# Optimization experiments

Hardware: AMD Instinct MI355X
Metric: run time of the kernel (lower is better)

The kernel has to match this reference:

```python
import jax, jax.numpy as jnp
import numpy as np
from jax import lax
from jax.scipy.special import logsumexp

B, T, Lc = 64, 512, 16
DW, CD, NF, KS, H, K, CV = 300, 50, 100, 3, 256, 9, 100
SCALE = 0.05


def setup_inputs() -> dict:
    key = jax.random.key(0)
    ks = jax.random.split(key, 20)
    f32 = jnp.float32
    return {
        'word_embs': jax.random.normal(ks[0], (B, T, DW), f32),
        'chars': jax.random.randint(ks[1], (B, T, Lc), 0, CV),
        'lengths': jax.random.randint(ks[2], (B,), T // 2, T + 1).astype(jnp.int32),
        'tags': jax.random.randint(ks[3], (B, T), 0, K),
        'fin_W': jax.random.normal(ks[4], (DW, DW), f32) * SCALE,
        'fin_b': jnp.zeros((DW,), f32),
        'char_emb': jax.random.normal(ks[5], (CV, CD), f32) * SCALE,
        'conv_W': jax.random.normal(ks[6], (KS, CD, NF), f32) * SCALE,  # (W, In, Out)
        'conv_b': jnp.zeros((NF,), f32),
        'Wih_f': jax.random.normal(ks[7], (4 * H, DW + NF), f32) * SCALE,
        'Whh_f': jax.random.normal(ks[8], (4 * H, H), f32) * SCALE,
        'b_f': jnp.zeros((4 * H,), f32),
        'Wih_b': jax.random.normal(ks[9], (4 * H, DW + NF), f32) * SCALE,
        'Whh_b': jax.random.normal(ks[10], (4 * H, H), f32) * SCALE,
        'b_b': jnp.zeros((4 * H,), f32),
        'out_W': jax.random.normal(ks[11], (2 * H, K), f32) * SCALE,
        'out_b': jnp.zeros((K,), f32),
        'trans': jax.random.normal(ks[12], (K, K), f32) * SCALE,
        'start_trans': jax.random.normal(ks[13], (K,), f32) * SCALE,
        'end_trans': jax.random.normal(ks[14], (K,), f32) * SCALE,
    }


def _lstm_scan(x, mask, Wih, Whh, b):
    # x: [B,T,D], mask: [B,T] bool -> outputs [B,T,H] (zeros at padding)
    xT = jnp.swapaxes(x, 0, 1)              # [T,B,D]
    mT = jnp.swapaxes(mask, 0, 1)           # [T,B]
    pre = jnp.einsum('tbd,gd->tbg', xT, Wih) + b  # precompute input part [T,B,4H]
    h0 = jnp.zeros((x.shape[0], Whh.shape[1]), x.dtype)

    def step(carry, inp):
        h, c = carry
        px, m = inp
        g = px + h @ Whh.T
        i, f, gg, o = jnp.split(g, 4, axis=-1)  # pytorch gate order i,f,g,o
        c_new = jax.nn.sigmoid(f) * c + jax.nn.sigmoid(i) * jnp.tanh(gg)
        h_new = jax.nn.sigmoid(o) * jnp.tanh(c_new)
        m = m[:, None]
        h2 = jnp.where(m, h_new, h)
        c2 = jnp.where(m, c_new, c)
        return (h2, c2), h2 * m

    _, hs = lax.scan(step, (h0, h0), (pre, mT))
    return jnp.swapaxes(hs, 0, 1)


def _reverse_by_length(x, lengths):
    # reverse the valid prefix of each sequence (padding stays at the end)
    t = jnp.arange(x.shape[1])
    rev = jnp.where(t[None, :] < lengths[:, None], lengths[:, None] - 1 - t[None, :], t[None, :])
    return jnp.take_along_axis(x, rev[:, :, None], axis=1)


def _crf_forward(logits, tags, mask, trans, start_trans, end_trans):
    # torchcrf-style log-likelihood; returns scalar sum over batch
    eT = jnp.swapaxes(logits, 0, 1)  # [T,B,K]
    mT = jnp.swapaxes(mask, 0, 1).astype(logits.dtype)  # [T,B]
    bidx = jnp.arange(logits.shape[0])
    # numerator: gold path score
    score = start_trans[tags[:, 0]] + eT[0][bidx, tags[:, 0]]

    def nstep(carry, inp):
        sc, prev = carry
        e, tg, m = inp
        step_sc = trans[prev, tg] + e[bidx, tg]
        sc = sc + m * step_sc
        prev = jnp.where(m > 0, tg, prev)
        return (sc, prev), None

    tT = jnp.swapaxes(tags, 0, 1)
    (score, last_tag), _ = lax.scan(nstep, (score, tags[:, 0]), (eT[1:], tT[1:], mT[1:]))
    score = score + end_trans[last_tag]
    # denominator: log-partition via forward algorithm
    alpha = start_trans[None, :] + eT[0]

    def fstep(a, inp):
        e, m = inp
        nxt = logsumexp(a[:, :, None] + trans[None, :, :] + e[:, None, :], axis=1)
        return jnp.where(m[:, None] > 0, nxt, a), None

    alpha, _ = lax.scan(fstep, alpha, (eT[1:], mT[1:]))
    Z = logsumexp(alpha + end_trans[None, :], axis=-1)
    return jnp.sum(score - Z)


def _viterbi(logits, mask, trans, start_trans, end_trans):
    eT = jnp.swapaxes(logits, 0, 1)  # [T,B,K]
    mT = jnp.swapaxes(mask, 0, 1)    # [T,B] bool
    Ktags = logits.shape[-1]
    ident = jnp.arange(Ktags)[None, :]

    def vstep(a, inp):
        e, m = inp
        cand = a[:, :, None] + trans[None, :, :]   # [B, K_prev, K_cur]
        bp = jnp.argmax(cand, axis=1)
        nxt = jnp.max(cand, axis=1) + e
        a2 = jnp.where(m[:, None], nxt, a)
        bp = jnp.where(m[:, None], bp, ident)       # identity backptr at padding
        return a2, bp

    alpha, bps = lax.scan(vstep, start_trans[None, :] + eT[0], (eT[1:], mT[1:]))
    last = jnp.argmax(alpha + end_trans[None, :], axis=-1)

    def bstep(tag, bp):
        prev = jnp.take_along_axis(bp, tag[:, None], axis=1)[:, 0]
        return prev, tag

    tag0, tail = lax.scan(bstep, last, bps, reverse=True)  # tail[t] = tag at time t+1
    path = jnp.concatenate([tag0[:, None], jnp.swapaxes(tail, 0, 1)], axis=1)  # [B,T]
    return path * mask  # zero-pad like zero_pad(preds)


def reference(word_embs, chars, lengths, tags, fin_W, fin_b, char_emb, conv_W, conv_b,
              Wih_f, Whh_f, b_f, Wih_b, Whh_b, b_b, out_W, out_b,
              trans, start_trans, end_trans):
    mask = jnp.arange(T)[None, :] < lengths[:, None]  # [B,T]
    # 1) word embeddings through finetune linear
    we = word_embs @ fin_W.T + fin_b
    # 2) char CNN: embed -> conv1d over chars -> relu -> max-pool
    ce = char_emb[chars].reshape(B * T, Lc, CD)
    conv = lax.conv_general_dilated(ce, conv_W, (1,), 'SAME',
                                    dimension_numbers=('NWC', 'WIO', 'NWC')) + conv_b
    char_feat = jnp.max(jax.nn.relu(conv), axis=1).reshape(B, T, NF)
    # 3) concat; 4) BiLSTM (dropout=0 / eval mode)
    x = jnp.concatenate([we, char_feat], axis=-1)
    h_fwd = _lstm_scan(x, mask, Wih_f, Whh_f, b_f)
    x_rev = _reverse_by_length(x, lengths)
    h_bwd = _reverse_by_length(_lstm_scan(x_rev, mask, Wih_b, Whh_b, b_b), lengths)
    lstm_out = jnp.concatenate([h_fwd, h_bwd], axis=-1)  # [B,T,2H]
    # 5) linear head; 6-7) CRF loss + viterbi decode
    logits = lstm_out @ out_W + out_b  # [B,T,K]
    loss = -_crf_forward(logits, tags, mask, trans, start_trans, end_trans)
    preds = _viterbi(logits, mask, trans, start_trans, end_trans)
    return loss, preds
```

## Files before the change

### kernel.cpp

```cpp
#include <hip/hip_runtime.h>


__device__ __forceinline__ float sigf(float x){ return 1.0f/(1.0f + expf(-x)); }

__global__ void pack_weights(const float* __restrict__ Wih_f, const float* __restrict__ Wih_b,
                             const float* __restrict__ Whh_f, const float* __restrict__ Whh_b,
                             const float* __restrict__ fin_W,
                             float4* __restrict__ Wp_f, float4* __restrict__ Wp_b,
                             float4* __restrict__ WT_f, float4* __restrict__ WT_b,
                             float* __restrict__ finWT){
  int stride = gridDim.x*blockDim.x;
  for (int idx = blockIdx.x*blockDim.x + threadIdx.x; idx < 425872; idx += stride){
    if (idx < 204800){
      int i2 = idx; const float* W = Wih_f; float4* P = Wp_f;
      if (i2 >= 102400){ i2 -= 102400; W = Wih_b; P = Wp_b; }
      int d = i2 >> 8, j = i2 & 255;
      P[i2] = make_float4(W[j*400+d], W[(j+256)*400+d], W[(j+512)*400+d], W[(j+768)*400+d]);
    } else if (idx < 335872){
      int i2 = idx - 204800; const float* W = Whh_f; float4* P = WT_f;
      if (i2 >= 65536){ i2 -= 65536; W = Whh_b; P = WT_b; }
      int d = i2 >> 8, j = i2 & 255;
      P[i2] = make_float4(W[j*256+d], W[(j+256)*256+d], W[(j+512)*256+d], W[(j+768)*256+d]);
    } else {
      int i2 = idx - 335872;
      int d = i2 / 300, j = i2 - d*300;
      finWT[d*304 + j] = fin_W[j*300 + d];
    }
  }
}

__global__ __launch_bounds__(256) void featurize(const float* __restrict__ we_in,
      const float* __restrict__ finWT, const float* __restrict__ finb,
      const int* __restrict__ chars, const float* __restrict__ char_emb,
      const float* __restrict__ convW, const float* __restrict__ convb,
      float* __restrict__ x){
  __shared__ __align__(16) char fsm[31104];
  int bid = blockIdx.x;
  int tid = threadIdx.x;
  if (bid < 2048){
    float* embT = (float*)fsm;
    int tok0 = bid * 16;
    for (int idx = tid; idx < 4800; idx += 256){
      int tt = idx / 300, d = idx - tt*300;
      embT[d*16 + tt] = we_in[(size_t)tok0*300 + idx];
    }
    __syncthreads();
    for (int j = tid; j < 300; j += 256){
      float bias = finb[j];
      float acc[16];
#pragma unroll
      for (int k2=0;k2<16;k2++) acc[k2]=bias;
      const float4* e4 = (const float4*)embT;
#pragma unroll 4
      for (int d=0; d<300; d++){
        float w = finWT[d*304 + j];
        float4 a = e4[d*4+0], b2 = e4[d*4+1], c2 = e4[d*4+2], d2 = e4[d*4+3];
        acc[0]+=a.x*w;  acc[1]+=a.y*w;  acc[2]+=a.z*w;  acc[3]+=a.w*w;
        acc[4]+=b2.x*w; acc[5]+=b2.y*w; acc[6]+=b2.z*w; acc[7]+=b2.w*w;
        acc[8]+=c2.x*w; acc[9]+=c2.y*w; acc[10]+=c2.z*w;acc[11]+=c2.w*w;
        acc[12]+=d2.x*w;acc[13]+=d2.y*w;acc[14]+=d2.z*w;acc[15]+=d2.w*w;
      }
#pragma unroll
      for (int k2=0;k2<16;k2++) x[(size_t)(tok0+k2)*400 + j] = acc[k2];
    }
  } else {
    float* ce2 = (float*)fsm;
    int* chs = (int*)(fsm + 30464);
    int tok0 = (bid - 2048) * 8;
    if (tid < 128) chs[tid] = chars[(size_t)tok0*16 + tid];
    __syncthreads();
    for (int idx = tid; idx < 7200; idx += 256){
      int tok = idx / 900; int r = idx - tok*900;
      int w1 = r / 50; int c = r - w1*50;
      float v = 0.f;
      if (w1 >= 1 && w1 <= 16) v = char_emb[chs[tok*16 + (w1-1)]*50 + c];
      ce2[tok*952 + c*19 + w1] = v;
    }
    __syncthreads();
    for (int p = tid; p < 800; p += 256){
      int tok = p / 100, f = p - tok*100;
      float s[16];
#pragma unroll
      for (int w=0; w<16; w++) s[w] = 0.f;
      const float* cebase = ce2 + tok*952;
      for (int c=0; c<50; c++){
        float cr[18];
#pragma unroll
        for (int i=0;i<18;i++) cr[i] = cebase[c*19+i];
#pragma unroll
        for (int k2=0;k2<3;k2++){
          float wv = convW[(k2*50+c)*100 + f];
#pragma unroll
          for (int w=0;w<16;w++) s[w] += cr[w+k2]*wv;
        }
      }
      float m = s[0];
#pragma unroll
      for (int w=1;w<16;w++) m = fmaxf(m, s[w]);
      m = fmaxf(0.f, m + convb[f]);
      x[(size_t)(tok0+tok)*400 + 300 + f] = m;
    }
  }
}

__global__ __launch_bounds__(256) void pre_gemm(const float* __restrict__ x,
     const float4* __restrict__ Wp_f, const float4* __restrict__ Wp_b,
     const float* __restrict__ b_f, const float* __restrict__ b_b,
     const int* __restrict__ lengths,
     float4* __restrict__ pre_f, float4* __restrict__ pre_b,
     int t0, int log2CH){
  int dir = blockIdx.z;
  const float4* Wp = dir ? Wp_b : Wp_f;
  const float* bias = dir ? b_b : b_f;
  float4* pre = dir ? pre_b : pre_f;
  int tok0 = blockIdx.x * 64;
  int j0 = blockIdx.y * 64;
  __shared__ float As[16][68];
  __shared__ float4 Bs[4][16][16];
  __shared__ int rows_s[64];
  int tid = threadIdx.x;
  int tx = tid & 15, ty = tid >> 4;
  int chm = (1 << log2CH) - 1;
  if (tid < 64){
    int tok = tok0 + tid;
    int b = tok >> log2CH;
    int trel = tok & chm;
    int t = t0 + trel;
    int row;
    if (dir == 0) row = t;
    else { int len = lengths[b]; int pr = len - 1 - t; row = pr < 0 ? 0 : pr; }
    rows_s[tid] = b*512 + row;
  }
  float4 acc[4][4];
#pragma unroll
  for (int s2=0;s2<4;s2++){
    int j = j0 + tx*4 + s2;
    float4 bj = make_float4(bias[j], bias[j+256], bias[j+512], bias[j+768]);
#pragma unroll
    for (int r=0;r<4;r++) acc[r][s2] = bj;
  }
  __syncthreads();
  int tokA = tid >> 2, kqA = tid & 3;
  int jjB = tid & 63,  kbB = tid >> 6;
  float4 aReg; float4 bReg[4];
  {
    aReg = *(const float4*)&x[(size_t)rows_s[tokA]*400 + 0 + kqA*4];
#pragma unroll
    for (int rr=0;rr<4;rr++) bReg[rr] = Wp[(size_t)(0 + kbB + rr*4)*256 + j0 + jjB];
  }
  for (int kt=0; kt<25; ++kt){
    As[kqA*4+0][tokA] = aReg.x;
    As[kqA*4+1][tokA] = aReg.y;
    As[kqA*4+2][tokA] = aReg.z;
    As[kqA*4+3][tokA] = aReg.w;
#pragma unroll
    for (int rr=0;rr<4;rr++) Bs[jjB&3][kbB+rr*4][jjB>>2] = bReg[rr];
    __syncthreads();
    if (kt < 24){
      int k0n = (kt+1)*16;
      aReg = *(const float4*)&x[(size_t)rows_s[tokA]*400 + k0n + kqA*4];
#pragma unroll
      for (int rr=0;rr<4;rr++) bReg[rr] = Wp[(size_t)(k0n + kbB + rr*4)*256 + j0 + jjB];
    }
#pragma unroll
    for (int kk=0; kk<16; ++kk){
      float a[4];
#pragma unroll
      for (int r=0;r<4;r++) a[r] = As[kk][ty*4+r];
#pragma unroll
      for (int s2=0;s2<4;s2++){
        float4 b4 = Bs[s2][kk][tx];
#pragma unroll
        for (int r=0;r<4;r++){
          acc[r][s2].x += a[r]*b4.x;
          acc[r][s2].y += a[r]*b4.y;
          acc[r][s2].z += a[r]*b4.z;
          acc[r][s2].w += a[r]*b4.w;
        }
      }
    }
    __syncthreads();
  }
#pragma unroll
  for (int r=0;r<4;r++){
    int tok = tok0 + ty*4 + r;
    int bb = tok >> log2CH;
    int tr = tok & chm;
#pragma unroll
    for (int s2=0;s2<4;s2++){
      pre[(size_t)(bb*128 + tr)*256 + j0 + tx*4 + s2] = acc[r][s2];
    }
  }
}

#define NRD 24
#define NLD 8
#define NSTREAM (64 - NRD - NLD)

#define OFF_WLDS 0
#define OFF_PART 131072
#define OFF_OWS  143360
#define OFF_H    152576
#define POOL_SZ  154624
#define PG_AS    0
#define PG_BS    4352
#define PG_ROWS  12544
#define PG_STRIDE 12800

__global__ __attribute__((amdgpu_num_vgpr(128))) __launch_bounds__(1024, 1)
void fused_scan_pre(const float4* __restrict__ prec_f, const float4* __restrict__ prec_b,
     const float4* __restrict__ pren_f, float4* __restrict__ pren_f_w,
     float4* __restrict__ pren_b_w,
     const float4* __restrict__ WT_f, const float4* __restrict__ WT_b,
     const float4* __restrict__ Wp_f, const float4* __restrict__ Wp_b,
     const float* __restrict__ b_f, const float* __restrict__ b_b,
     const float* __restrict__ x, const int* __restrict__ lengths,
     const float* __restrict__ outW,
     float* __restrict__ logits_f, float* __restrict__ logits_b,
     float* __restrict__ st_h, float* __restrict__ st_c,
     int t0, int nsteps, int t0n, int do_pre){
  __shared__ __align__(16) char smem[POOL_SZ];
  int wid = blockIdx.x;
  int tid = threadIdx.x;
  if (wid < 128){
    int dir = wid & 1;
    int b = wid >> 1;
    int len = lengths[b];
    if (len <= t0) return;
    const float4* pre = (dir ? prec_b : prec_f) + (size_t)b*128*256;
    const float4* WT = dir ? WT_b : WT_f;
    float* lg = (dir ? logits_b : logits_f) + (size_t)b*512*9;
    float4* wlds = (float4*)(smem + OFF_WLDS);
    float4* part = (float4*)(smem + OFF_PART);
    float*  oWs  = (float*)(smem + OFF_OWS);
    float*  hbuf = (float*)(smem + OFF_H);
    int j = tid & 255, q = tid >> 8;
    for (int i = tid; i < 2304; i += 1024) oWs[i] = outW[dir*2304 + i];
    for (int i = tid; i < 4*NLD*256; i += 1024){
      int qq = i >> 11;
      int rr = i & (NLD*256 - 1);
      int dl = rr >> 8, jj = rr & 255;
      wlds[(qq*NLD + dl)*256 + jj] = WT[(size_t)(qq*64 + NRD + dl)*256 + jj];
    }
    const float4* WTq = WT + (size_t)q*64*256;
    float4 wreg[NRD];
#pragma unroll
    for (int r=0; r<NRD; ++r) wreg[r] = WTq[(size_t)r*256 + j];
    float c = 0.f;
    if (t0 == 0){
      if (tid < 256) hbuf[tid] = 0.f;
    } else {
      if (tid < 256) hbuf[tid] = st_h[(dir*64+b)*256 + tid];
      if (q == 0) c = st_c[(dir*64+b)*256 + j];
    }
    __syncthreads();
    int tend = len < t0+nsteps ? len : t0+nsteps;
    const float4* WTs = WTq + (size_t)(NRD+NLD)*256 + j;
    int cur = 0;
    for (int t=t0; t<tend; ++t){
      const float* hc = hbuf + (cur << 8);
      const float* hq = hc + (q << 6);
      float4 p0;
      if (q == 0) p0 = pre[(size_t)(t - t0)*256 + j];
      float4 acc = make_float4(0.f,0.f,0.f,0.f);
#pragma unroll 8
      for (int s=0; s<NSTREAM; ++s){
        float hv = hq[NRD+NLD+s];
        float4 w = WTs[(size_t)s*256];
        acc.x += w.x*hv; acc.y += w.y*hv; acc.z += w.z*hv; acc.w += w.w*hv;
      }
#pragma unroll
      for (int r=0; r<NRD; ++r){
        float hv = hq[r];
        float4 w = wreg[r];
        acc.x += w.x*hv; acc.y += w.y*hv; acc.z += w.z*hv; acc.w += w.w*hv;
      }
#pragma unroll
      for (int l=0; l<NLD; ++l){
        float hv = hq[NRD+l];
        float4 w = wlds[(q*NLD + l)*256 + j];
        acc.x += w.x*hv; acc.y += w.y*hv; acc.z += w.z*hv; acc.w += w.w*hv;
      }
      if (q) part[((q-1)<<8) + j] = acc;
      if (t > t0 && tid < 576){
        int pprev = dir ? (len - t) : (t - 1);
        int k = tid >> 6, l = tid & 63;
        float s = hc[l]*oWs[l*9+k] + hc[l+64]*oWs[(l+64)*9+k]
                + hc[l+128]*oWs[(l+128)*9+k] + hc[l+192]*oWs[(l+192)*9+k];
#pragma unroll
        for (int o=32; o; o>>=1) s += __shfl_down(s, o, 64);
        if (l == 0) lg[pprev*9 + k] = s;
      }
      __syncthreads();
      if (q == 0){
        float4 p1 = part[j], p2 = part[256+j], p3 = part[512+j];
        float gi = acc.x + p0.x + p1.x + p2.x + p3.x;
        float gf = acc.y + p0.y + p1.y + p2.y + p3.y;
        float gg = acc.z + p0.z + p1.z + p2.z + p3.z;
        float go = acc.w + p0.w + p1.w + p2.w + p3.w;
        c = sigf(gf)*c + sigf(gi)*tanhf(gg);
        float h = sigf(go)*tanhf(c);
        hbuf[((cur^1)<<8) + j] = h;
      }
      __syncthreads();
      cur ^= 1;
    }
    const float* hc = hbuf + (cur << 8);
    if (tid < 576){
      int plast = dir ? (len - tend) : (tend - 1);
      int k = tid >> 6, l = tid & 63;
      float s = hc[l]*oWs[l*9+k] + hc[l+64]*oWs[(l+64)*9+k]
              + hc[l+128]*oWs[(l+128)*9+k] + hc[l+192]*oWs[(l+192)*9+k];
#pragma unroll
      for (int o=32; o; o>>=1) s += __shfl_down(s, o, 64);
      if (l == 0) lg[plast*9 + k] = s;
    }
    if (tid < 256) st_h[(dir*64+b)*256 + tid] = hc[tid];
    if (q == 0) st_c[(dir*64+b)*256 + j] = c;
  } else {
    if (!do_pre) return;
    int w = wid - 128;
    int g = tid >> 8, lt = tid & 255;
    char* gp = smem + g*PG_STRIDE;
    float (*As)[68] = (float(*)[68])(gp + PG_AS);
    float4* Bsl = (float4*)(gp + PG_BS);
    int* rows = (int*)(gp + PG_ROWS);
    int tx = lt & 15, ty4 = (lt >> 4) * 4;
    int tokA = lt >> 2, kqA = lt & 3;
    int uB = lt & 31, kbB = lt >> 5;
    for (int s=0; s<4; ++s){
      int tix = s*512 + g*128 + w;
      int dir = tix & 1;
      int jh = (tix >> 1) & 7;
      int tokT = tix >> 4;
      int j0u = jh * 32;
      int tok0 = tokT * 64;
      const float4* Wp = dir ? Wp_b : Wp_f;
      const float* bias = dir ? b_b : b_f;
      float4* pren = dir ? pren_b_w : pren_f_w;
      __syncthreads();
      if (lt < 64){
        int tok = tok0 + lt;
        int bb = tok >> 7, trel = tok & 127;
        int t = t0n + trel; if (t > 511) t = 511;
        int row;
        if (dir == 0) row = t;
        else { int len = lengths[bb]; int pr = len - 1 - t; row = pr < 0 ? 0 : pr; }
        rows[lt] = bb*512 + row;
      }
      float4 acc[4][2];
#pragma unroll
      for (int s2=0;s2<2;s2++){
        int u = j0u + tx + s2*16;
        float4 bj = make_float4(bias[u], bias[u+256], bias[u+512], bias[u+768]);
#pragma unroll
        for (int r=0;r<4;r++) acc[r][s2] = bj;
      }
      __syncthreads();
      for (int kt=0; kt<25; ++kt){
        int k0 = kt*16;
        {
          const float* xr = x + (size_t)rows[tokA]*400 + k0 + kqA*4;
          float4 av = *(const float4*)xr;
          As[kqA*4+0][tokA]=av.x; As[kqA*4+1][tokA]=av.y;
          As[kqA*4+2][tokA]=av.z; As[kqA*4+3][tokA]=av.w;
          Bsl[kbB*32 + uB]     = Wp[(size_t)(k0+kbB)*256 + j0u + uB];
          Bsl[(kbB+8)*32 + uB] = Wp[(size_t)(k0+kbB+8)*256 + j0u + uB];
        }
        __syncthreads();
#pragma unroll 4
        for (int kk=0; kk<16; ++kk){
          float a0 = As[kk][ty4+0], a1 = As[kk][ty4+1], a2 = As[kk][ty4+2], a3 = As[kk][ty4+3];
          float4 b0 = Bsl[kk*32 + tx], b1 = Bsl[kk*32 + tx + 16];
          acc[0][0].x += a0*b0.x; acc[0][0].y += a0*b0.y; acc[0][0].z += a0*b0.z; acc[0][0].w += a0*b0.w;
          acc[1][0].x += a1*b0.x; acc[1][0].y += a1*b0.y; acc[1][0].z += a1*b0.z; acc[1][0].w += a1*b0.w;
          acc[2][0].x += a2*b0.x; acc[2][0].y += a2*b0.y; acc[2][0].z += a2*b0.z; acc[2][0].w += a2*b0.w;
          acc[3][0].x += a3*b0.x; acc[3][0].y += a3*b0.y; acc[3][0].z += a3*b0.z; acc[3][0].w += a3*b0.w;
          acc[0][1].x += a0*b1.x; acc[0][1].y += a0*b1.y; acc[0][1].z += a0*b1.z; acc[0][1].w += a0*b1.w;
          acc[1][1].x += a1*b1.x; acc[1][1].y += a1*b1.y; acc[1][1].z += a1*b1.z; acc[1][1].w += a1*b1.w;
          acc[2][1].x += a2*b1.x; acc[2][1].y += a2*b1.y; acc[2][1].z += a2*b1.z; acc[2][1].w += a2*b1.w;
          acc[3][1].x += a3*b1.x; acc[3][1].y += a3*b1.y; acc[3][1].z += a3*b1.z; acc[3][1].w += a3*b1.w;
        }
        __syncthreads();
      }
#pragma unroll
      for (int r=0;r<4;r++){
        int tok = tok0 + ty4 + r;
        pren[(size_t)tok*256 + j0u + tx]      = acc[r][0];
        pren[(size_t)tok*256 + j0u + tx + 16] = acc[r][1];
      }
    }
  }
}

__global__ __launch_bounds__(64) void crf_viterbi_kernel(const float* __restrict__ logits_f,
     const float* __restrict__ logits_b, const float* __restrict__ outb_,
     const int* __restrict__ tags, const int* __restrict__ lengths,
     const float* __restrict__ trans, const float* __restrict__ start_trans,
     const float* __restrict__ end_trans, float* __restrict__ loss_partial,
     float* __restrict__ preds){
  int wid = blockIdx.x;
  int is_crf = wid < 64 ? 1 : 0;
  int b = is_crf ? wid : wid - 64;
  int len = lengths[b];
  int tid = threadIdx.x;
  __shared__ float e_s[4608];
  __shared__ float tr[81];
  __shared__ float alpha[9];
  __shared__ int tg[512];
  __shared__ unsigned char bp[4608];
  const float* lf = logits_f + (size_t)b*4608;
  const float* lb = logits_b + (size_t)b*4608;
  for (int i=tid; i<4608; i+=64){
    int k = i - (i/9)*9;
    e_s[i] = lf[i] + lb[i] + outb_[k];
  }
  for (int i=tid; i<81; i+=64) tr[i] = trans[i];
  if (is_crf){
    for (int i=tid; i<512; i+=64) tg[i] = tags[b*512 + i];
    __syncthreads();
    if (tid < 9) alpha[tid] = start_trans[tid] + e_s[tid];
    __syncthreads();
    for (int t=1; t<len; ++t){
      float nxt = 0.f;
      if (tid < 9){
        float v[9];
#pragma unroll
        for (int j2=0;j2<9;j2++) v[j2] = alpha[j2] + tr[j2*9+tid];
        float m = v[0];
#pragma unroll
        for (int j2=1;j2<9;j2++) m = fmaxf(m, v[j2]);
        float ssum = 0.f;
#pragma unroll
        for (int j2=0;j2<9;j2++) ssum += expf(v[j2]-m);
        nxt = m + logf(ssum) + e_s[t*9+tid];
      }
      __syncthreads();
      if (tid < 9) alpha[tid] = nxt;
      __syncthreads();
    }
    if (tid == 0){
      float m = alpha[0] + end_trans[0];
      for (int k2=1;k2<9;k2++) m = fmaxf(m, alpha[k2]+end_trans[k2]);
      float ssum = 0.f;
      for (int k2=0;k2<9;k2++) ssum += expf(alpha[k2]+end_trans[k2]-m);
      float Z = m + logf(ssum);
      int prev = tg[0];
      float sc = start_trans[prev] + e_s[prev];
      for (int t=1;t<len;++t){
        int cur = tg[t];
        sc += tr[prev*9+cur] + e_s[t*9+cur];
        prev = cur;
      }
      sc += end_trans[prev];
      loss_partial[b] = Z - sc;
    }
  } else {
    __syncthreads();
    if (tid < 9) alpha[tid] = start_trans[tid] + e_s[tid];
    __syncthreads();
    for (int t=1; t<len; ++t){
      float nxt = 0.f; int bj = 0;
      if (tid < 9){
        float m = alpha[0] + tr[tid];
#pragma unroll
        for (int j2=1;j2<9;j2++){
          float v = alpha[j2] + tr[j2*9+tid];
          if (v > m){ m = v; bj = j2; }
        }
        nxt = m + e_s[t*9+tid];
      }
      __syncthreads();
      if (tid < 9){ alpha[tid] = nxt; bp[t*9+tid] = (unsigned char)bj; }
      __syncthreads();
    }
    for (int p2 = len + tid; p2 < 512; p2 += 64) preds[(size_t)b*512 + p2] = 0.f;
    if (tid == 0){
      float m = alpha[0] + end_trans[0]; int last = 0;
      for (int k2=1;k2<9;k2++){
        float v = alpha[k2] + end_trans[k2];
        if (v > m){ m = v; last = k2; }
      }
      int cur = last;
      preds[(size_t)b*512 + (len-1)] = (float)cur;
      for (int p2 = len-2; p2 >= 0; --p2){
        cur = bp[(p2+1)*9 + cur];
        preds[(size_t)b*512 + p2] = (float)cur;
      }
    }
  }
}

__global__ void loss_sum_kernel(const float* __restrict__ lp, float* __restrict__ out){
  float v = lp[threadIdx.x];
#pragma unroll
  for (int o=32; o; o>>=1) v += __shfl_down(v, o, 64);
  if (threadIdx.x == 0) out[0] = v;
}

extern "C" void kernel_launch(void* const* d_in, const int* in_sizes, int n_in,
                              void* d_out, int out_size, void* d_ws, size_t ws_size,
                              hipStream_t stream) {
  const float* word_embs  = (const float*)d_in[0];
  const int*   chars      = (const int*)  d_in[1];
  const int*   lengths    = (const int*)  d_in[2];
  const int*   tags       = (const int*)  d_in[3];
  const float* fin_W      = (const float*)d_in[4];
  const float* fin_b      = (const float*)d_in[5];
  const float* char_emb   = (const float*)d_in[6];
  const float* conv_W     = (const float*)d_in[7];
  const float* conv_b     = (const float*)d_in[8];
  const float* Wih_f      = (const float*)d_in[9];
  const float* Whh_f      = (const float*)d_in[10];
  const float* b_f        = (const float*)d_in[11];
  const float* Wih_b      = (const float*)d_in[12];
  const float* Whh_b      = (const float*)d_in[13];
  const float* b_b        = (const float*)d_in[14];
  const float* out_W      = (const float*)d_in[15];
  const float* out_b      = (const float*)d_in[16];
  const float* trans      = (const float*)d_in[17];
  const float* start_tr   = (const float*)d_in[18];
  const float* end_tr     = (const float*)d_in[19];

  float* ws = (float*)d_ws;
  float*  x         = ws;
  float4* Wp_f      = (float4*)(ws + 13107200);
  float4* Wp_b      = (float4*)(ws + 13516800);
  float4* WT_f      = (float4*)(ws + 13926400);
  float4* WT_b      = (float4*)(ws + 14188544);
  float*  finWT     = ws + 14450688;
  float*  logits_f  = ws + 14541888;
  float*  logits_b  = ws + 14836800;
  float*  st_h      = ws + 15131712;
  float*  st_c      = ws + 15164480;
  float*  loss_part = ws + 15197248;
  const size_t FIXED_F = 15197312;
  float4* preA_f = (float4*)(ws + FIXED_F);
  float4* preA_b = preA_f + (size_t)64*128*256;
  float4* preB_f = preA_b + (size_t)64*128*256;
  float4* preB_b = preB_f + (size_t)64*128*256;

  float* out = (float*)d_out;

  pack_weights<<<1664, 256, 0, stream>>>(Wih_f, Wih_b, Whh_f, Whh_b, fin_W,
                                         Wp_f, Wp_b, WT_f, WT_b, finWT);
  featurize<<<6144, 256, 0, stream>>>(word_embs, finWT, fin_b, chars, char_emb,
                                      conv_W, conv_b, x);

  pre_gemm<<<dim3(32, 4, 2), 256, 0, stream>>>(x, Wp_f, Wp_b, b_f, b_b, lengths,
                                               preA_f, preA_b, 0, 5);
  fused_scan_pre<<<256, 1024, 0, stream>>>(preA_f, preA_b, preB_f, preB_f, preB_b,
      WT_f, WT_b, Wp_f, Wp_b, b_f, b_b, x, lengths, out_W,
      logits_f, logits_b, st_h, st_c, 0, 32, 32, 1);
  fused_scan_pre<<<256, 1024, 0, stream>>>(preB_f, preB_b, preA_f, preA_f, preA_b,
      WT_f, WT_b, Wp_f, Wp_b, b_f, b_b, x, lengths, out_W,
      logits_f, logits_b, st_h, st_c, 32, 128, 160, 1);
  fused_scan_pre<<<256, 1024, 0, stream>>>(preA_f, preA_b, preB_f, preB_f, preB_b,
      WT_f, WT_b, Wp_f, Wp_b, b_f, b_b, x, lengths, out_W,
      logits_f, logits_b, st_h, st_c, 160, 128, 288, 1);
  fused_scan_pre<<<256, 1024, 0, stream>>>(preB_f, preB_b, preA_f, preA_f, preA_b,
      WT_f, WT_b, Wp_f, Wp_b, b_f, b_b, x, lengths, out_W,
      logits_f, logits_b, st_h, st_c, 288, 128, 416, 1);
  fused_scan_pre<<<256, 1024, 0, stream>>>(preA_f, preA_b, preB_f, preB_f, preB_b,
      WT_f, WT_b, Wp_f, Wp_b, b_f, b_b, x, lengths, out_W,
      logits_f, logits_b, st_h, st_c, 416, 96, 0, 0);

  crf_viterbi_kernel<<<128, 64, 0, stream>>>(logits_f, logits_b, out_b, tags, lengths,
                                             trans, start_tr, end_tr, loss_part, out + 1);
  loss_sum_kernel<<<1, 64, 0, stream>>>(loss_part, out);
}
```

Measured before the change: 3.887 ms.

## Rebalance LSTM scan chunks so precompute GEMM hides behind each scan segment

Replaces the uneven 32/128/128/128/96 time-chunk schedule with six roughly equal 85/86-step chunks. The next chunk's input-projection GEMM now runs on the spare blocks during every scan launch instead of being exposed at the start, and works with chunk sizes that are not powers of two through an explicit output-position table. It also vectorises the shared-memory A-operand reads and drops the forced 128-VGPR cap on the fused kernel. The cost is an extra kernel launch, integer division in the index math, and a possible register-pressure change.

```diff
diff --git a/kernel.cpp b/kernel.cpp
--- a/kernel.cpp
+++ b/kernel.cpp
@@ -108,7 +108,7 @@
      const float* __restrict__ b_f, const float* __restrict__ b_b,
      const int* __restrict__ lengths,
      float4* __restrict__ pre_f, float4* __restrict__ pre_b,
-     int t0, int log2CH){
+     int t0, int CH){
   int dir = blockIdx.z;
   const float4* Wp = dir ? Wp_b : Wp_f;
   const float* bias = dir ? b_b : b_f;
@@ -118,18 +118,19 @@
   __shared__ float As[16][68];
   __shared__ float4 Bs[4][16][16];
   __shared__ int rows_s[64];
+  __shared__ int poss_s[64];
   int tid = threadIdx.x;
   int tx = tid & 15, ty = tid >> 4;
-  int chm = (1 << log2CH) - 1;
   if (tid < 64){
     int tok = tok0 + tid;
-    int b = tok >> log2CH;
-    int trel = tok & chm;
+    int b = tok / CH;
+    int trel = tok - b*CH;
     int t = t0 + trel;
     int row;
     if (dir == 0) row = t;
     else { int len = lengths[b]; int pr = len - 1 - t; row = pr < 0 ? 0 : pr; }
     rows_s[tid] = b*512 + row;
+    poss_s[tid] = b*128 + trel;
   }
   float4 acc[4][4];
 #pragma unroll
@@ -164,9 +165,8 @@
     }
 #pragma unroll
     for (int kk=0; kk<16; ++kk){
-      float a[4];
-#pragma unroll
-      for (int r=0;r<4;r++) a[r] = As[kk][ty*4+r];
+      float4 a4 = *(const float4*)&As[kk][ty*4];
+      float a[4] = {a4.x, a4.y, a4.z, a4.w};
 #pragma unroll
       for (int s2=0;s2<4;s2++){
         float4 b4 = Bs[s2][kk][tx];
@@ -183,12 +183,10 @@
   }
 #pragma unroll
   for (int r=0;r<4;r++){
-    int tok = tok0 + ty*4 + r;
-    int bb = tok >> log2CH;
-    int tr = tok & chm;
+    int pp = poss_s[ty*4+r];
 #pragma unroll
     for (int s2=0;s2<4;s2++){
-      pre[(size_t)(bb*128 + tr)*256 + j0 + tx*4 + s2] = acc[r][s2];
+      pre[(size_t)pp*256 + j0 + tx*4 + s2] = acc[r][s2];
     }
   }
 }
@@ -205,12 +203,11 @@
 #define PG_AS    0
 #define PG_BS    4352
 #define PG_ROWS  12544
-#define PG_STRIDE 12800
-
-__global__ __attribute__((amdgpu_num_vgpr(128))) __launch_bounds__(1024, 1)
+#define PG_STRIDE 13056
+
+__global__ __launch_bounds__(1024, 1)
 void fused_scan_pre(const float4* __restrict__ prec_f, const float4* __restrict__ prec_b,
-     const float4* __restrict__ pren_f, float4* __restrict__ pren_f_w,
-     float4* __restrict__ pren_b_w,
+     float4* __restrict__ pren_f_w, float4* __restrict__ pren_b_w,
      const float4* __restrict__ WT_f, const float4* __restrict__ WT_b,
      const float4* __restrict__ Wp_f, const float4* __restrict__ Wp_b,
      const float* __restrict__ b_f, const float* __restrict__ b_b,
@@ -218,7 +215,7 @@
      const float* __restrict__ outW,
      float* __restrict__ logits_f, float* __restrict__ logits_b,
      float* __restrict__ st_h, float* __restrict__ st_c,
-     int t0, int nsteps, int t0n, int do_pre){
+     int t0, int nsteps, int t0n, int cnext, int do_pre){
   __shared__ __align__(16) char smem[POOL_SZ];
   int wid = blockIdx.x;
   int tid = threadIdx.x;
@@ -325,11 +322,15 @@
     float (*As)[68] = (float(*)[68])(gp + PG_AS);
     float4* Bsl = (float4*)(gp + PG_BS);
     int* rows = (int*)(gp + PG_ROWS);
+    int* poss = rows + 64;
     int tx = lt & 15, ty4 = (lt >> 4) * 4;
     int tokA = lt >> 2, kqA = lt & 3;
     int uB = lt & 31, kbB = lt >> 5;
-    for (int s=0; s<4; ++s){
+    int tixmax = cnext << 4;
+    int smax = (tixmax + 511) >> 9;
+    for (int s=0; s<smax; ++s){
       int tix = s*512 + g*128 + w;
+      bool active = tix < tixmax;
       int dir = tix & 1;
       int jh = (tix >> 1) & 7;
       int tokT = tix >> 4;
@@ -339,14 +340,16 @@
       const float* bias = dir ? b_b : b_f;
       float4* pren = dir ? pren_b_w : pren_f_w;
       __syncthreads();
-      if (lt < 64){
+      if (active && lt < 64){
         int tok = tok0 + lt;
-        int bb = tok >> 7, trel = tok & 127;
-        int t = t0n + trel; if (t > 511) t = 511;
+        int bb = tok / cnext;
+        int trel = tok - bb*cnext;
+        int t = t0n + trel;
         int row;
         if (dir == 0) row = t;
         else { int len = lengths[bb]; int pr = len - 1 - t; row = pr < 0 ? 0 : pr; }
         rows[lt] = bb*512 + row;
+        poss[lt] = bb*128 + trel;
       }
       float4 acc[4][2];
 #pragma unroll
@@ -359,7 +362,7 @@
       __syncthreads();
       for (int kt=0; kt<25; ++kt){
         int k0 = kt*16;
-        {
+        if (active){
           const float* xr = x + (size_t)rows[tokA]*400 + k0 + kqA*4;
           float4 av = *(const float4*)xr;
           As[kqA*4+0][tokA]=av.x; As[kqA*4+1][tokA]=av.y;
@@ -368,26 +371,31 @@
           Bsl[(kbB+8)*32 + uB] = Wp[(size_t)(k0+kbB+8)*256 + j0u + uB];
         }
         __syncthreads();
+        if (active){
 #pragma unroll 4
-        for (int kk=0; kk<16; ++kk){
-          float a0 = As[kk][ty4+0], a1 = As[kk][ty4+1], a2 = As[kk][ty4+2], a3 = As[kk][ty4+3];
-          float4 b0 = Bsl[kk*32 + tx], b1 = Bsl[kk*32 + tx + 16];
-          acc[0][0].x += a0*b0.x; acc[0][0].y += a0*b0.y; acc[0][0].z += a0*b0.z; acc[0][0].w += a0*b0.w;
-          acc[1][0].x += a1*b0.x; acc[1][0].y += a1*b0.y; acc[1][0].z += a1*b0.z; acc[1][0].w += a1*b0.w;
-          acc[2][0].x += a2*b0.x; acc[2][0].y += a2*b0.y; acc[2][0].z += a2*b0.z; acc[2][0].w += a2*b0.w;
-          acc[3][0].x += a3*b0.x; acc[3][0].y += a3*b0.y; acc[3][0].z += a3*b0.z; acc[3][0].w += a3*b0.w;
-          acc[0][1].x += a0*b1.x; acc[0][1].y += a0*b1.y; acc[0][1].z += a0*b1.z; acc[0][1].w += a0*b1.w;
-          acc[1][1].x += a1*b1.x; acc[1][1].y += a1*b1.y; acc[1][1].z += a1*b1.z; acc[1][1].w += a1*b1.w;
-          acc[2][1].x += a2*b1.x; acc[2][1].y += a2*b1.y; acc[2][1].z += a2*b1.z; acc[2][1].w += a2*b1.w;
-          acc[3][1].x += a3*b1.x; acc[3][1].y += a3*b1.y; acc[3][1].z += a3*b1.z; acc[3][1].w += a3*b1.w;
+          for (int kk=0; kk<16; ++kk){
+            float4 a4 = *(const float4*)&As[kk][ty4];
+            float a0 = a4.x, a1 = a4.y, a2 = a4.z, a3 = a4.w;
+            float4 b0 = Bsl[kk*32 + tx], b1 = Bsl[kk*32 + tx + 16];
+            acc[0][0].x += a0*b0.x; acc[0][0].y += a0*b0.y; acc[0][0].z += a0*b0.z; acc[0][0].w += a0*b0.w;
+            acc[1][0].x += a1*b0.x; acc[1][0].y += a1*b0.y; acc[1][0].z += a1*b0.z; acc[1][0].w += a1*b0.w;
+            acc[2][0].x += a2*b0.x; acc[2][0].y += a2*b0.y; acc[2][0].z += a2*b0.z; acc[2][0].w += a2*b0.w;
+            acc[3][0].x += a3*b0.x; acc[3][0].y += a3*b0.y; acc[3][0].z += a3*b0.z; acc[3][0].w += a3*b0.w;
+            acc[0][1].x += a0*b1.x; acc[0][1].y += a0*b1.y; acc[0][1].z += a0*b1.z; acc[0][1].w += a0*b1.w;
+            acc[1][1].x += a1*b1.x; acc[1][1].y += a1*b1.y; acc[1][1].z += a1*b1.z; acc[1][1].w += a1*b1.w;
+            acc[2][1].x += a2*b1.x; acc[2][1].y += a2*b1.y; acc[2][1].z += a2*b1.z; acc[2][1].w += a2*b1.w;
+            acc[3][1].x += a3*b1.x; acc[3][1].y += a3*b1.y; acc[3][1].z += a3*b1.z; acc[3][1].w += a3*b1.w;
+          }
         }
         __syncthreads();
       }
-#pragma unroll
-      for (int r=0;r<4;r++){
-        int tok = tok0 + ty4 + r;
-        pren[(size_t)tok*256 + j0u + tx]      = acc[r][0];
-        pren[(size_t)tok*256 + j0u + tx + 16] = acc[r][1];
+      if (active){
+#pragma unroll
+        for (int r=0;r<4;r++){
+          int pp = poss[ty4 + r];
+          pren[(size_t)pp*256 + j0u + tx]      = acc[r][0];
+          pren[(size_t)pp*256 + j0u + tx + 16] = acc[r][1];
+        }
       }
     }
   }
@@ -547,23 +555,26 @@
   featurize<<<6144, 256, 0, stream>>>(word_embs, finWT, fin_b, chars, char_emb,
                                       conv_W, conv_b, x);
 
-  pre_gemm<<<dim3(32, 4, 2), 256, 0, stream>>>(x, Wp_f, Wp_b, b_f, b_b, lengths,
-                                               preA_f, preA_b, 0, 5);
-  fused_scan_pre<<<256, 1024, 0, stream>>>(preA_f, preA_b, preB_f, preB_f, preB_b,
+  pre_gemm<<<dim3(86, 4, 2), 256, 0, stream>>>(x, Wp_f, Wp_b, b_f, b_b, lengths,
+                                               preA_f, preA_b, 0, 86);
+  fused_scan_pre<<<256, 1024, 0, stream>>>(preA_f, preA_b, preB_f, preB_b,
       WT_f, WT_b, Wp_f, Wp_b, b_f, b_b, x, lengths, out_W,
-      logits_f, logits_b, st_h, st_c, 0, 32, 32, 1);
-  fused_scan_pre<<<256, 1024, 0, stream>>>(preB_f, preB_b, preA_f, preA_f, preA_b,
+      logits_f, logits_b, st_h, st_c, 0, 86, 86, 86, 1);
+  fused_scan_pre<<<256, 1024, 0, stream>>>(preB_f, preB_b, preA_f, preA_b,
       WT_f, WT_b, Wp_f, Wp_b, b_f, b_b, x, lengths, out_W,
-      logits_f, logits_b, st_h, st_c, 32, 128, 160, 1);
-  fused_scan_pre<<<256, 1024, 0, stream>>>(preA_f, preA_b, preB_f, preB_f, preB_b,
+      logits_f, logits_b, st_h, st_c, 86, 86, 172, 85, 1);
+  fused_scan_pre<<<256, 1024, 0, stream>>>(preA_f, preA_b, preB_f, preB_b,
       WT_f, WT_b, Wp_f, Wp_b, b_f, b_b, x, lengths, out_W,
-      logits_f, logits_b, st_h, st_c, 160, 128, 288, 1);
-  fused_scan_pre<<<256, 1024, 0, stream>>>(preB_f, preB_b, preA_f, preA_f, preA_b,
+      logits_f, logits_b, st_h, st_c, 172, 85, 257, 85, 1);
+  fused_scan_pre<<<256, 1024, 0, stream>>>(preB_f, preB_b, preA_f, preA_b,
       WT_f, WT_b, Wp_f, Wp_b, b_f, b_b, x, lengths, out_W,
-      logits_f, logits_b, st_h, st_c, 288, 128, 416, 1);
-  fused_scan_pre<<<256, 1024, 0, stream>>>(preA_f, preA_b, preB_f, preB_f, preB_b,
+      logits_f, logits_b, st_h, st_c, 257, 85, 342, 85, 1);
+  fused_scan_pre<<<256, 1024, 0, stream>>>(preA_f, preA_b, preB_f, preB_b,
       WT_f, WT_b, Wp_f, Wp_b, b_f, b_b, x, lengths, out_W,
-      logits_f, logits_b, st_h, st_c, 416, 96, 0, 0);
+      logits_f, logits_b, st_h, st_c, 342, 85, 427, 85, 1);
+  fused_scan_pre<<<256, 1024, 0, stream>>>(preB_f, preB_b, preA_f, preA_b,
+      WT_f, WT_b, Wp_f, Wp_b, b_f, b_b, x, lengths, out_W,
+      logits_f, logits_b, st_h, st_c, 427, 85, 0, 85, 0);
 
   crf_viterbi_kernel<<<128, 64, 0, stream>>>(logits_f, logits_b, out_b, tags, lengths,
                                              trans, start_tr, end_tr, loss_part, out + 1);
```

Measured after the change: 3.821 ms (median of 2 runs). No clear change (-1.7%).
